# Kernel optimization log

Measured on AMD Instinct MI355X. Metric: run time of the kernel, lower is better.

The kernel has to match this reference:

```python
import jax, jax.numpy as jnp
import numpy as np

B, S, DIM = 2, 2048, 2048
NH, NKV = 32, 8
HD = DIM // NH          # 64
NREP = NH // NKV        # 4
BASE = 10000.0


def setup_inputs() -> dict:
    key = jax.random.key(0)
    ks = jax.random.split(key, 5)
    x = jax.random.normal(ks[0], (B, S, DIM), dtype=jnp.float32)
    # causal mask, 1 = keep, 0 = masked (matches masked_fill(mask == 0, -inf))
    mask = jnp.tril(jnp.ones((S, S), dtype=jnp.float32))[None, None]
    scale = 0.02
    Wq = jax.random.normal(ks[1], (DIM, NH * HD), dtype=jnp.float32) * scale
    Wk = jax.random.normal(ks[2], (DIM, NKV * HD), dtype=jnp.float32) * scale
    Wv = jax.random.normal(ks[3], (DIM, NKV * HD), dtype=jnp.float32) * scale
    Wo = jax.random.normal(ks[4], (NH * HD, DIM), dtype=jnp.float32) * scale
    return {"x": x, "mask": mask, "Wq": Wq, "Wk": Wk, "Wv": Wv, "Wo": Wo}


def _rope_cos_sin(seq_len, head_dim, dtype):
    inv_freq = 1.0 / (BASE ** (jnp.arange(0, head_dim, 2, dtype=jnp.float32) / head_dim))
    t = jnp.arange(seq_len, dtype=jnp.float32)
    freqs = t[:, None] * inv_freq[None, :]            # [S, HD/2]
    return jnp.cos(freqs).astype(dtype), jnp.sin(freqs).astype(dtype)


def _apply_rope(x, cos, sin):
    # x: [B, H, S, HD]; cos/sin: [S, HD/2] broadcast over B,H
    x1, x2 = jnp.split(x, 2, axis=-1)
    c = cos[None, None]
    s = sin[None, None]
    return jnp.concatenate([x1 * c - x2 * s, x2 * c + x1 * s], axis=-1)


def reference(x, mask, Wq, Wk, Wv, Wo):
    b, s, _ = x.shape
    q = (x @ Wq).reshape(b, s, NH, HD).transpose(0, 2, 1, 3)   # [B,NH,S,HD]
    k = (x @ Wk).reshape(b, s, NKV, HD).transpose(0, 2, 1, 3)  # [B,NKV,S,HD]
    v = (x @ Wv).reshape(b, s, NKV, HD).transpose(0, 2, 1, 3)
    cos, sin = _rope_cos_sin(s, HD, x.dtype)
    q = _apply_rope(q, cos, sin)
    k = _apply_rope(k, cos, sin)
    # GQA: repeat kv heads
    k = jnp.repeat(k, NREP, axis=1)
    v = jnp.repeat(v, NREP, axis=1)
    scale = HD ** -0.5
    attn = jnp.einsum('bhqd,bhkd->bhqk', q, k) * scale
    attn = jnp.where(mask == 0, -jnp.inf, attn)
    attn = jax.nn.softmax(attn, axis=-1)
    out = jnp.einsum('bhqk,bhkd->bhqd', attn, v)
    out = out.transpose(0, 2, 1, 3).reshape(b, s, NH * HD)
    return out @ Wo
```

## Files before the change

kernel.cpp:

```cpp
#include <hip/hip_runtime.h>
#include <stdint.h>

typedef __attribute__((ext_vector_type(8))) short short8;
typedef __attribute__((ext_vector_type(4))) short short4v;
typedef __attribute__((ext_vector_type(4))) float float4v;
typedef __attribute__((ext_vector_type(16))) float f32x16;
typedef __attribute__((ext_vector_type(4))) int int4v;
typedef __attribute__((ext_vector_type(2))) int int2v;
typedef __attribute__((ext_vector_type(2))) unsigned int uint2v;

#define DEV __device__ __forceinline__

DEV ushort f2bf(float f){
  uint32_t u = __float_as_uint(f);
  u = (u + 0x7fffu + ((u >> 16) & 1u)) >> 16;
  return (ushort)u;
}
DEV float bf2f(ushort h){
  uint32_t u = ((uint32_t)h) << 16;
  return __uint_as_float(u);
}

DEV void gload16(const void* g, void* l){
  __builtin_amdgcn_global_load_lds((const __attribute__((address_space(1))) void*)g,
                                   (__attribute__((address_space(3))) void*)l, 16, 0, 0);
}

DEV uint32_t cvtpk(float lo, float hi){
  uint32_t d;
  asm("v_cvt_pk_bf16_f32 %0, %1, %2" : "=v"(d) : "v"(lo), "v"(hi));
  return d;
}

DEV uint2v plswap2(uint32_t a, uint32_t b){
  return __builtin_amdgcn_permlane32_swap(a, b, false, false);
}

__global__ __launch_bounds__(256) void k_prep(const float* __restrict__ x, const float* __restrict__ Wq,
                                              const float* __restrict__ Wk, const float* __restrict__ Wv,
                                              const float* __restrict__ Wo,
                                              ushort* __restrict__ xb, ushort* __restrict__ wqkvt,
                                              ushort* __restrict__ wot,
                                              float* __restrict__ cost, float* __restrict__ sint,
                                              float qscale){
  __shared__ float tile[32][33];
  const int bid = blockIdx.x;
  if (bid < 10240){
    const float* src; ushort* dst; int N, K, bx, by; float scale;
    if (bid < 4096){ src = Wq; dst = wqkvt; N = 2048; K = 2048; scale = qscale; bx = bid & 63; by = bid >> 6; }
    else if (bid < 5120){ int lb = bid - 4096; src = Wk; dst = wqkvt + (size_t)2048 * 2048; N = 512; K = 2048; scale = 1.f; bx = lb & 15; by = lb >> 4; }
    else if (bid < 6144){ int lb = bid - 5120; src = Wv; dst = wqkvt + (size_t)2560 * 2048; N = 512; K = 2048; scale = 1.f; bx = lb & 15; by = lb >> 4; }
    else { int lb = bid - 6144; src = Wo; dst = wot; N = 2048; K = 2048; scale = 1.f; bx = lb & 63; by = lb >> 6; }
    int c0 = bx * 32, r0 = by * 32;
    int tx = threadIdx.x & 31, ty = threadIdx.x >> 5;
    #pragma unroll
    for (int i = 0; i < 32; i += 8)
      tile[ty + i][tx] = src[(size_t)(r0 + ty + i) * N + (c0 + tx)];
    __syncthreads();
    #pragma unroll
    for (int i = 0; i < 32; i += 8)
      dst[(size_t)(c0 + ty + i) * K + (r0 + tx)] = f2bf(tile[tx][ty + i] * scale);
  } else if (bid < 10496){
    int i = (bid - 10240) * 256 + threadIdx.x;
    int s = i >> 5, d = i & 31;
    float inv = powf(10000.0f, -(float)d / 32.0f);
    float ang = (float)s * inv;
    float sv, cv;
    sincosf(ang, &sv, &cv);
    cost[i] = cv;
    sint[i] = sv;
  } else {
    int i = (bid - 10496) * 256 + threadIdx.x;
    float4v v = *(const float4v*)(x + (size_t)i * 4);
    short4v o;
    o[0] = (short)f2bf(v[0]); o[1] = (short)f2bf(v[1]);
    o[2] = (short)f2bf(v[2]); o[3] = (short)f2bf(v[3]);
    *(short4v*)(xb + (size_t)i * 4) = o;
  }
}

template<int BM, int BN, bool OUTF32, int MINW>
__global__ __launch_bounds__(512, MINW) void k_gemm8(const ushort* __restrict__ A, const ushort* __restrict__ Bt,
                                                     void* __restrict__ Cp, int M, int N, int K, int nbx){
  constexpr int WM = BM / 2, WN = BN / 4;
  constexpr int MR = WM / 16, NR = WN / 16, MP = MR / 4;
  constexpr int AISS = BM / 64, BISS = BN / 64;
  constexpr int BUFB = (BM + BN) * 128;
  __shared__ char lds[2 * BUFB];

  int wg = blockIdx.x;
  int cpx = (int)gridDim.x >> 3;
  wg = (wg & 7) * cpx + (wg >> 3);
  const int bn = wg % nbx, bm = wg / nbx;
  const int tid = threadIdx.x;
  const int w = tid >> 6, l = tid & 63, l15 = l & 15, hi = l >> 4;
  const int wr = w >> 2, wc = w & 3;

  const int r8 = tid >> 3;
  const int ce = ((tid & 7) ^ (r8 & 7)) << 3;
  const ushort* ag = A + (size_t)(bm * BM + r8) * K + ce;
  const ushort* bg = Bt + (size_t)(bn * BN + r8) * K + ce;

  float4v acc[MR][NR];
  #pragma unroll
  for (int a = 0; a < MR; ++a)
    #pragma unroll
    for (int b = 0; b < NR; ++b)
      acc[a][b] = (float4v){0.f, 0.f, 0.f, 0.f};

  auto stage = [&](int kt, int buf){
    char* ab = lds + buf * BUFB;
    char* bb = ab + BM * 128;
    #pragma unroll
    for (int i = 0; i < AISS; ++i)
      gload16(ag + (size_t)(i * 64) * K + kt * 64, ab + i * 8192 + tid * 16);
    #pragma unroll
    for (int i = 0; i < BISS; ++i)
      gload16(bg + (size_t)(i * 64) * K + kt * 64, bb + i * 8192 + tid * 16);
  };
  auto lda = [&](const char* ab, int mf, int kk)->short8{
    int row = wr * WM + mf * 16 + l15;
    int a = (row * 128 + kk * 64 + hi * 16) ^ ((row & 7) << 4);
    return *(const short8*)(ab + a);
  };
  auto ldb = [&](const char* bb, int nf, int kk)->short8{
    int row = wc * WN + nf * 16 + l15;
    int a = (row * 128 + kk * 64 + hi * 16) ^ ((row & 7) << 4);
    return *(const short8*)(bb + a);
  };

  const int nkt = K >> 6;
  stage(0, 0);
  for (int t = 0; t < nkt; ++t){
    asm volatile("s_waitcnt vmcnt(0)" ::: "memory");
    __builtin_amdgcn_s_barrier();
    __builtin_amdgcn_sched_barrier(0);
    if (t + 1 < nkt) stage(t + 1, (t + 1) & 1);

    const char* ab = lds + (t & 1) * BUFB;
    const char* bb = ab + BM * 128;
    short8 bfr[NR][2];
    #pragma unroll
    for (int nf = 0; nf < NR; ++nf){ bfr[nf][0] = ldb(bb, nf, 0); bfr[nf][1] = ldb(bb, nf, 1); }
    short8 af[MP][2];
    #pragma unroll
    for (int ml = 0; ml < MP; ++ml){ af[ml][0] = lda(ab, ml, 0); af[ml][1] = lda(ab, ml, 1); }

    #pragma unroll
    for (int p = 0; p < 4; ++p){
      asm volatile("s_waitcnt lgkmcnt(0)" ::: "memory");
      __builtin_amdgcn_sched_barrier(0);
      __builtin_amdgcn_s_setprio(1);
      #pragma unroll
      for (int ml = 0; ml < MP; ++ml)
        #pragma unroll
        for (int nf = 0; nf < NR; ++nf){
          const int mf = p * MP + ml;
          acc[mf][nf] = __builtin_amdgcn_mfma_f32_16x16x32_bf16(af[ml][0], bfr[nf][0], acc[mf][nf], 0, 0, 0);
          acc[mf][nf] = __builtin_amdgcn_mfma_f32_16x16x32_bf16(af[ml][1], bfr[nf][1], acc[mf][nf], 0, 0, 0);
        }
      __builtin_amdgcn_s_setprio(0);
      __builtin_amdgcn_sched_barrier(0);
      if (p < 3){
        #pragma unroll
        for (int ml = 0; ml < MP; ++ml){
          af[ml][0] = lda(ab, (p + 1) * MP + ml, 0);
          af[ml][1] = lda(ab, (p + 1) * MP + ml, 1);
        }
      }
    }
  }

  #pragma unroll
  for (int mf = 0; mf < MR; ++mf){
    int row0 = bm * BM + wr * WM + mf * 16 + hi * 4;
    #pragma unroll
    for (int nf = 0; nf < NR; ++nf){
      int col = bn * BN + wc * WN + nf * 16 + l15;
      #pragma unroll
      for (int reg = 0; reg < 4; ++reg){
        size_t idx = (size_t)(row0 + reg) * N + col;
        if constexpr (OUTF32) ((float*)Cp)[idx] = acc[mf][nf][reg];
        else                  ((ushort*)Cp)[idx] = f2bf(acc[mf][nf][reg]);
      }
    }
  }
}

__global__ __launch_bounds__(256) void k_rope_vt(ushort* __restrict__ qkv, const float* __restrict__ cost,
                                                 const float* __restrict__ sint, ushort* __restrict__ vt){
  __shared__ ushort tile[64][72];
  const int bid = blockIdx.x;
  if (bid < 5120){
    int t = bid * 256 + threadIdx.x;
    int row = t / 320;
    int rem = t - row * 320;
    int head = rem >> 3, d0 = (rem & 7) * 4;
    int s = row & 2047;
    ushort* p = qkv + (size_t)row * 3072 + head * 64 + d0;
    short4v a = *(short4v*)p;
    short4v b = *(short4v*)(p + 32);
    float4v c  = *(const float4v*)(cost + s * 32 + d0);
    float4v sn = *(const float4v*)(sint + s * 32 + d0);
    short4v na, nb;
    #pragma unroll
    for (int j = 0; j < 4; ++j){
      float x1 = bf2f((ushort)a[j]), x2 = bf2f((ushort)b[j]);
      na[j] = (short)f2bf(x1 * c[j] - x2 * sn[j]);
      nb[j] = (short)f2bf(x2 * c[j] + x1 * sn[j]);
    }
    *(short4v*)p = na;
    *(short4v*)(p + 32) = nb;
  } else {
    int lb = bid - 5120;
    int g = lb >> 5, st = lb & 31;
    int b = g >> 3, hk = g & 7;
    const ushort* src = qkv + (size_t)(b * 2048 + st * 64) * 3072 + 2560 + hk * 64;
    int tid = threadIdx.x;
    #pragma unroll
    for (int i = 0; i < 2; ++i){
      int r = i * 32 + (tid >> 3), c8 = (tid & 7) * 8;
      short8 v = *(const short8*)(src + (size_t)r * 3072 + c8);
      #pragma unroll
      for (int j = 0; j < 8; ++j) tile[r][c8 + j] = (ushort)v[j];
    }
    __syncthreads();
    ushort* dst = vt + (size_t)g * 64 * 2048 + st * 64;
    #pragma unroll
    for (int i = 0; i < 2; ++i){
      int d = i * 32 + (tid >> 3), s8 = (tid & 7) * 8;
      short8 ov;
      #pragma unroll
      for (int j = 0; j < 8; ++j) ov[j] = (short)tile[s8 + j][d];
      *(short8*)(dst + (size_t)d * 2048 + s8) = ov;
    }
  }
}

__global__ __launch_bounds__(256) void k_attn8(const ushort* __restrict__ qkv, const ushort* __restrict__ vt,
                                               ushort* __restrict__ att){
  __shared__ __align__(16) char lds[2][16384];
  const int raw = blockIdx.x;
  const int xcd = raw & 7, slot = raw >> 3;
  const int qb = 15 - (slot >> 3);
  const int rem = slot & 7;
  const int gidx = xcd * 2 + (rem >> 2);
  const int b = gidx >> 3, hk = gidx & 7;
  const int h = hk * 4 + (rem & 3);
  const int tid = threadIdx.x;
  const int w = tid >> 6, l = tid & 63, ql = l & 31, g = l >> 5;
  const int qw = qb * 128 + w * 32;
  const int diag_t = (qw + 31) >> 6;
  const int swz = (ql & 7) << 4;

  short8 qf[4];
  {
    const ushort* qbase = qkv + (size_t)(b * 2048 + qw + ql) * 3072 + h * 64 + g * 8;
    #pragma unroll
    for (int ds = 0; ds < 4; ++ds) qf[ds] = *(const short8*)(qbase + ds * 16);
  }
  short8 onesf;
  #pragma unroll
  for (int i = 0; i < 8; ++i) onesf[i] = (short)0x3F80;

  f32x16 o0, o1, ladd;
  #pragma unroll
  for (int r = 0; r < 16; ++r){ o0[r] = 0.f; o1[r] = 0.f; ladd[r] = 0.f; }

  const int srow = tid >> 3;
  const int ce = ((tid & 7) ^ (srow & 7)) << 3;
  const ushort* kg = qkv + (size_t)(b * 2048 + srow) * 3072 + 2048 + hk * 64 + ce;
  const ushort* vg = vt + (size_t)gidx * 64 * 2048 + (size_t)srow * 2048 + ce;
  const int nt = qb * 2 + 2;

  auto stage = [&](int t, int buf){
    char* lb = lds[buf];
    #pragma unroll
    for (int i = 0; i < 2; ++i)
      gload16(kg + (size_t)(t * 64 + i * 32) * 3072, lb + i * 4096 + tid * 16);
    #pragma unroll
    for (int i = 0; i < 2; ++i)
      gload16(vg + (size_t)(i * 32) * 2048 + t * 64, lb + 8192 + i * 4096 + tid * 16);
  };

  stage(0, 0);
  for (int t = 0; t < nt; ++t){
    asm volatile("s_waitcnt vmcnt(0)" ::: "memory");
    __builtin_amdgcn_s_barrier();
    __builtin_amdgcn_sched_barrier(0);
    if (t + 1 < nt) stage(t + 1, (t + 1) & 1);

    if (t <= diag_t){
      const char* Kb = lds[t & 1];
      const char* Vb = Kb + 8192;

      f32x16 sa0, sa1;
      #pragma unroll
      for (int r = 0; r < 16; ++r){ sa0[r] = 0.f; sa1[r] = 0.f; }
      __builtin_amdgcn_s_setprio(1);
      #pragma unroll
      for (int ds = 0; ds < 4; ++ds){
        int cb = (ds * 32 + g * 16) ^ swz;
        short8 k0 = *(const short8*)(Kb + ql * 128 + cb);
        short8 k1 = *(const short8*)(Kb + (32 + ql) * 128 + cb);
        sa0 = __builtin_amdgcn_mfma_f32_32x32x16_bf16(k0, qf[ds], sa0, 0, 0, 0);
        sa1 = __builtin_amdgcn_mfma_f32_32x32x16_bf16(k1, qf[ds], sa1, 0, 0, 0);
      }
      __builtin_amdgcn_s_setprio(0);

      if (t == diag_t){
        int thr = qw + ql - t * 64;
        #pragma unroll
        for (int r = 0; r < 16; ++r){
          int kl = (r & 3) + 8 * (r >> 2) + 4 * g;
          sa0[r] = (kl > thr) ? -3e38f : sa0[r];
          sa1[r] = (kl + 32 > thr) ? -3e38f : sa1[r];
        }
      }

      uint32_t wds[2][8];
      #pragma unroll
      for (int u = 0; u < 8; ++u){
        float a0 = __builtin_amdgcn_exp2f(sa0[2 * u]);
        float a1 = __builtin_amdgcn_exp2f(sa0[2 * u + 1]);
        wds[0][u] = cvtpk(a0, a1);
        float b0 = __builtin_amdgcn_exp2f(sa1[2 * u]);
        float b1 = __builtin_amdgcn_exp2f(sa1[2 * u + 1]);
        wds[1][u] = cvtpk(b0, b1);
      }

      __builtin_amdgcn_s_setprio(1);
      #pragma unroll
      for (int ks = 0; ks < 4; ++ks){
        const int s2 = ks >> 1, c4 = (ks & 1) * 4;
        uint2v e0 = plswap2(wds[s2][c4 + 0], wds[s2][c4 + 2]);
        uint2v e1 = plswap2(wds[s2][c4 + 1], wds[s2][c4 + 3]);
        union { int4v w4; short8 s8; } pb;
        pb.w4[0] = (int)e0[0]; pb.w4[1] = (int)e1[0];
        pb.w4[2] = (int)e0[1]; pb.w4[3] = (int)e1[1];
        int cb = (ks * 32 + g * 16) ^ swz;
        short8 v0 = *(const short8*)(Vb + ql * 128 + cb);
        short8 v1 = *(const short8*)(Vb + (32 + ql) * 128 + cb);
        o0 = __builtin_amdgcn_mfma_f32_32x32x16_bf16(v0, pb.s8, o0, 0, 0, 0);
        o1 = __builtin_amdgcn_mfma_f32_32x32x16_bf16(v1, pb.s8, o1, 0, 0, 0);
        ladd = __builtin_amdgcn_mfma_f32_32x32x16_bf16(onesf, pb.s8, ladd, 0, 0, 0);
      }
      __builtin_amdgcn_s_setprio(0);
    }
  }

  float invl = 1.0f / ladd[0];
  ushort* ob = att + (size_t)(b * 2048 + qw + ql) * 2048 + h * 64;
  #pragma unroll
  for (int dm = 0; dm < 2; ++dm){
    #pragma unroll
    for (int rg = 0; rg < 4; ++rg){
      float f0 = (dm ? o1[4 * rg + 0] : o0[4 * rg + 0]) * invl;
      float f1 = (dm ? o1[4 * rg + 1] : o0[4 * rg + 1]) * invl;
      float f2 = (dm ? o1[4 * rg + 2] : o0[4 * rg + 2]) * invl;
      float f3 = (dm ? o1[4 * rg + 3] : o0[4 * rg + 3]) * invl;
      int2v wv;
      wv[0] = (int)cvtpk(f0, f1);
      wv[1] = (int)cvtpk(f2, f3);
      int d0 = dm * 32 + 8 * rg + 4 * g;
      *(int2v*)(ob + d0) = wv;
    }
  }
}

extern "C" void kernel_launch(void* const* d_in, const int* in_sizes, int n_in,
                              void* d_out, int out_size, void* d_ws, size_t ws_size,
                              hipStream_t stream) {
  const float* x  = (const float*)d_in[0];
  const float* Wq = (const float*)d_in[2];
  const float* Wk = (const float*)d_in[3];
  const float* Wv = (const float*)d_in[4];
  const float* Wo = (const float*)d_in[5];

  char* ws = (char*)d_ws;
  ushort* xb    = (ushort*)(ws);
  ushort* wqkvt = (ushort*)(ws + (16u << 20));
  ushort* wot   = (ushort*)(ws + (28u << 20));
  ushort* qkv   = (ushort*)(ws + (36u << 20));
  ushort* att   = (ushort*)(ws + (60u << 20));
  ushort* vt    = (ushort*)(ws + (76u << 20));
  float*  cost  = (float*)(ws + (80u << 20));
  float*  sint  = (float*)(ws + (80u << 20) + 262144);

  const float qscale = 0.125f * 1.4426950408889634f;

  k_prep<<<18688, 256, 0, stream>>>(x, Wq, Wk, Wv, Wo, xb, wqkvt, wot, cost, sint, qscale);
  k_gemm8<128, 192, false, 4><<<512, 512, 0, stream>>>(xb, wqkvt, qkv, 4096, 3072, 2048, 16);
  k_rope_vt<<<5632, 256, 0, stream>>>(qkv, cost, sint, vt);
  k_attn8<<<1024, 256, 0, stream>>>(qkv, vt, att);
  k_gemm8<128, 128, true, 4><<<512, 512, 0, stream>>>(att, wot, d_out, 4096, 2048, 2048, 16);
}
```

Baseline: 167.7 us.

## Split long causal query blocks across two workgroups and combine partials

The attention kernel now splits the KV loop of the eight longest query blocks per head into two halves run by separate workgroups, writing unnormalised bf16 partial outputs and row sums to scratch space that reuses the x and weight buffers. A new combine kernel adds the partials and normalises them into the attention output. Shorter query blocks still run unsplit. This is meant to even out the causal work imbalance and raise parallelism, at the cost of an extra launch, extra memory traffic, and rounding the partials to bf16. Adding the partials without rescaling relies on the softmax max-handling already in the loop being consistent across the two halves.

```diff
diff --git a/kernel.cpp b/kernel.cpp
--- a/kernel.cpp
+++ b/kernel.cpp
@@ -237,16 +237,36 @@
   }
 }
 
-__global__ __launch_bounds__(256) void k_attn8(const ushort* __restrict__ qkv, const ushort* __restrict__ vt,
-                                               ushort* __restrict__ att){
+__global__ __launch_bounds__(256) void k_attn9(const ushort* __restrict__ qkv, const ushort* __restrict__ vt,
+                                               ushort* __restrict__ att,
+                                               ushort* __restrict__ pO, float* __restrict__ pl){
   __shared__ __align__(16) char lds[2][16384];
-  const int raw = blockIdx.x;
-  const int xcd = raw & 7, slot = raw >> 3;
-  const int qb = 15 - (slot >> 3);
-  const int rem = slot & 7;
-  const int gidx = xcd * 2 + (rem >> 2);
+  const int id = blockIdx.x;
+  int gidx, hloc, qb, t0, t1, slot = 0;
+  bool split;
+  if (id < 1024){
+    int xcd = id & 7, s2 = id >> 3;
+    gidx = xcd * 2 + (s2 >> 6);
+    int idx6 = s2 & 63;
+    hloc = idx6 & 3;
+    int c = (idx6 >> 2) & 1;
+    qb = 15 - (idx6 >> 3);
+    int nt = 2 * qb + 2, hh = nt >> 1;
+    t0 = c * hh; t1 = t0 + hh;
+    split = true;
+    slot = (((gidx * 4 + hloc) * 8) + (15 - qb)) * 2 + c;
+  } else {
+    int id2 = id - 1024;
+    int xcd = id2 & 7, s3 = id2 >> 3;
+    gidx = xcd * 2 + (s3 & 1);
+    int idx5 = s3 >> 1;
+    hloc = idx5 & 3;
+    qb = 7 - (idx5 >> 2);
+    t0 = 0; t1 = 2 * qb + 2;
+    split = false;
+  }
   const int b = gidx >> 3, hk = gidx & 7;
-  const int h = hk * 4 + (rem & 3);
+  const int h = hk * 4 + hloc;
   const int tid = threadIdx.x;
   const int w = tid >> 6, l = tid & 63, ql = l & 31, g = l >> 5;
   const int qw = qb * 128 + w * 32;
@@ -271,7 +291,6 @@
   const int ce = ((tid & 7) ^ (srow & 7)) << 3;
   const ushort* kg = qkv + (size_t)(b * 2048 + srow) * 3072 + 2048 + hk * 64 + ce;
   const ushort* vg = vt + (size_t)gidx * 64 * 2048 + (size_t)srow * 2048 + ce;
-  const int nt = qb * 2 + 2;
 
   auto stage = [&](int t, int buf){
     char* lb = lds[buf];
@@ -283,12 +302,12 @@
       gload16(vg + (size_t)(i * 32) * 2048 + t * 64, lb + 8192 + i * 4096 + tid * 16);
   };
 
-  stage(0, 0);
-  for (int t = 0; t < nt; ++t){
+  stage(t0, t0 & 1);
+  for (int t = t0; t < t1; ++t){
     asm volatile("s_waitcnt vmcnt(0)" ::: "memory");
     __builtin_amdgcn_s_barrier();
     __builtin_amdgcn_sched_barrier(0);
-    if (t + 1 < nt) stage(t + 1, (t + 1) & 1);
+    if (t + 1 < t1) stage(t + 1, (t + 1) & 1);
 
     if (t <= diag_t){
       const char* Kb = lds[t & 1];
@@ -349,23 +368,75 @@
     }
   }
 
-  float invl = 1.0f / ladd[0];
-  ushort* ob = att + (size_t)(b * 2048 + qw + ql) * 2048 + h * 64;
+  if (split){
+    ushort* po = pO + (size_t)slot * 8192 + (size_t)(w * 32 + ql) * 64;
+    #pragma unroll
+    for (int dm = 0; dm < 2; ++dm){
+      #pragma unroll
+      for (int rg = 0; rg < 4; ++rg){
+        float f0 = dm ? o1[4 * rg + 0] : o0[4 * rg + 0];
+        float f1 = dm ? o1[4 * rg + 1] : o0[4 * rg + 1];
+        float f2 = dm ? o1[4 * rg + 2] : o0[4 * rg + 2];
+        float f3 = dm ? o1[4 * rg + 3] : o0[4 * rg + 3];
+        int2v wv;
+        wv[0] = (int)cvtpk(f0, f1);
+        wv[1] = (int)cvtpk(f2, f3);
+        *(int2v*)(po + dm * 32 + 8 * rg + 4 * g) = wv;
+      }
+    }
+    if (!g) pl[slot * 128 + w * 32 + ql] = ladd[0];
+  } else {
+    float invl = 1.0f / ladd[0];
+    ushort* ob = att + (size_t)(b * 2048 + qw + ql) * 2048 + h * 64;
+    #pragma unroll
+    for (int dm = 0; dm < 2; ++dm){
+      #pragma unroll
+      for (int rg = 0; rg < 4; ++rg){
+        float f0 = (dm ? o1[4 * rg + 0] : o0[4 * rg + 0]) * invl;
+        float f1 = (dm ? o1[4 * rg + 1] : o0[4 * rg + 1]) * invl;
+        float f2 = (dm ? o1[4 * rg + 2] : o0[4 * rg + 2]) * invl;
+        float f3 = (dm ? o1[4 * rg + 3] : o0[4 * rg + 3]) * invl;
+        int2v wv;
+        wv[0] = (int)cvtpk(f0, f1);
+        wv[1] = (int)cvtpk(f2, f3);
+        *(int2v*)(ob + dm * 32 + 8 * rg + 4 * g) = wv;
+      }
+    }
+  }
+}
+
+__global__ __launch_bounds__(256) void k_combine(const ushort* __restrict__ pO, const float* __restrict__ pl,
+                                                 ushort* __restrict__ att){
+  const int id = blockIdx.x;
+  const int pid = id >> 1, half = id & 1;
+  const int head = pid >> 3, qb8 = pid & 7;
+  const int qb = 15 - qb8;
+  const int gidx = head >> 2, hloc = head & 3;
+  const int b = gidx >> 3, hk = gidx & 7;
+  const int h = hk * 4 + hloc;
+  const int s0 = (head * 8 + qb8) * 2;
+  const int tid = threadIdx.x;
+  const int r = half * 64 + (tid >> 2);
+  const int cc = (tid & 3) * 16;
+  const ushort* A = pO + (size_t)s0 * 8192 + (size_t)r * 64 + cc;
+  const ushort* B = A + 8192;
+  float lsum = pl[s0 * 128 + r] + pl[(s0 + 1) * 128 + r];
+  float inv = 1.0f / lsum;
+  short8 xa0 = *(const short8*)A, xa1 = *(const short8*)(A + 8);
+  short8 xb0 = *(const short8*)B, xb1 = *(const short8*)(B + 8);
+  ushort* dst = att + (size_t)(b * 2048 + qb * 128 + r) * 2048 + h * 64 + cc;
+  int4v w0, w1;
   #pragma unroll
-  for (int dm = 0; dm < 2; ++dm){
-    #pragma unroll
-    for (int rg = 0; rg < 4; ++rg){
-      float f0 = (dm ? o1[4 * rg + 0] : o0[4 * rg + 0]) * invl;
-      float f1 = (dm ? o1[4 * rg + 1] : o0[4 * rg + 1]) * invl;
-      float f2 = (dm ? o1[4 * rg + 2] : o0[4 * rg + 2]) * invl;
-      float f3 = (dm ? o1[4 * rg + 3] : o0[4 * rg + 3]) * invl;
-      int2v wv;
-      wv[0] = (int)cvtpk(f0, f1);
-      wv[1] = (int)cvtpk(f2, f3);
-      int d0 = dm * 32 + 8 * rg + 4 * g;
-      *(int2v*)(ob + d0) = wv;
-    }
-  }
+  for (int j = 0; j < 4; ++j){
+    float e0 = (bf2f((ushort)xa0[2 * j]) + bf2f((ushort)xb0[2 * j])) * inv;
+    float e1 = (bf2f((ushort)xa0[2 * j + 1]) + bf2f((ushort)xb0[2 * j + 1])) * inv;
+    w0[j] = (int)cvtpk(e0, e1);
+    float e2 = (bf2f((ushort)xa1[2 * j]) + bf2f((ushort)xb1[2 * j])) * inv;
+    float e3 = (bf2f((ushort)xa1[2 * j + 1]) + bf2f((ushort)xb1[2 * j + 1])) * inv;
+    w1[j] = (int)cvtpk(e2, e3);
+  }
+  *(int4v*)dst = w0;
+  *(int4v*)(dst + 8) = w1;
 }
 
 extern "C" void kernel_launch(void* const* d_in, const int* in_sizes, int n_in,
@@ -387,11 +458,15 @@
   float*  cost  = (float*)(ws + (80u << 20));
   float*  sint  = (float*)(ws + (80u << 20) + 262144);
 
+  ushort* pO = xb;
+  float*  pl = (float*)wqkvt;
+
   const float qscale = 0.125f * 1.4426950408889634f;
 
   k_prep<<<18688, 256, 0, stream>>>(x, Wq, Wk, Wv, Wo, xb, wqkvt, wot, cost, sint, qscale);
   k_gemm8<128, 192, false, 4><<<512, 512, 0, stream>>>(xb, wqkvt, qkv, 4096, 3072, 2048, 16);
   k_rope_vt<<<5632, 256, 0, stream>>>(qkv, cost, sint, vt);
-  k_attn8<<<1024, 256, 0, stream>>>(qkv, vt, att);
+  k_attn9<<<1536, 256, 0, stream>>>(qkv, vt, att, pO, pl);
+  k_combine<<<1024, 256, 0, stream>>>(pO, pl, att);
   k_gemm8<128, 128, true, 4><<<512, 512, 0, stream>>>(att, wot, d_out, 4096, 2048, 2048, 16);
 }
```

New measurement: 176.7 us. 5.4% more time.
